# Kernel tuning notes

Measured on AMD Instinct MI355X. Metric: run time of the kernel, lower is better.

## Reference

```python
import jax, jax.numpy as jnp
import numpy as np

N = 50000
E = 800000
F_IN = 128
HID = 16
HEADS = 8
C = 16
NEG_SLOPE = 0.2


def setup_inputs() -> dict:
    key = jax.random.key(0)
    ks = jax.random.split(key, 12)
    glorot = lambda k, shape: jax.random.normal(k, shape, jnp.float32) * jnp.sqrt(2.0 / (shape[0] + shape[-1]))
    return {
        "x": jax.random.normal(ks[0], (N, F_IN), jnp.float32),
        "edge_index": jax.random.randint(ks[1], (2, E), 0, N, jnp.int32),
        "x2": jax.random.normal(ks[2], (N, F_IN), jnp.float32),
        "edge_index2": jax.random.randint(ks[3], (2, E), 0, N, jnp.int32),
        # conv1: GATConv(F_IN -> HID, heads=HEADS, concat=True)
        "W1": glorot(ks[4], (F_IN, HEADS * HID)),
        "a1_src": glorot(ks[5], (HEADS, HID)),
        "a1_dst": glorot(ks[6], (HEADS, HID)),
        "b1": jnp.zeros((HEADS * HID,), jnp.float32),
        # conv2: GATConv(HEADS*HID -> C, heads=1, concat=False)
        "W2": glorot(ks[7], (HEADS * HID, 1 * C)),
        "a2_src": glorot(ks[8], (1, C)),
        "a2_dst": glorot(ks[9], (1, C)),
        "b2": jnp.zeros((C,), jnp.float32),
    }


def gat_conv(x, edge_index, W, a_src, a_dst, bias, concat):
    """PyG-style GATConv with self-loops, segment softmax over destinations."""
    n = x.shape[0]
    heads, out = a_src.shape
    h = (x @ W).reshape(n, heads, out)               # [N, H, O]
    loops = jnp.arange(n, dtype=edge_index.dtype)
    src = jnp.concatenate([edge_index[0], loops])     # messages flow src -> dst
    dst = jnp.concatenate([edge_index[1], loops])
    alpha_s = jnp.einsum('nho,ho->nh', h, a_src)
    alpha_d = jnp.einsum('nho,ho->nh', h, a_dst)
    e = jax.nn.leaky_relu(alpha_s[src] + alpha_d[dst], NEG_SLOPE)  # [E+N, H]
    m = jax.lax.stop_gradient(jax.ops.segment_max(e, dst, num_segments=n))
    w = jnp.exp(e - m[dst])
    denom = jax.ops.segment_sum(w, dst, num_segments=n)
    alpha = w / (denom[dst] + 1e-16)                  # segment softmax
    msg = h[src] * alpha[:, :, None]                  # [E+N, H, O]
    agg = jax.ops.segment_sum(msg, dst, num_segments=n)
    agg = agg.reshape(n, heads * out) if concat else agg.mean(axis=1)
    return agg + bias


def forward_once(x, edge_index, W1, a1_src, a1_dst, b1, W2, a2_src, a2_dst, b2):
    # dropout(p=0.6) is identity in eval mode
    h = jax.nn.elu(gat_conv(x, edge_index, W1, a1_src, a1_dst, b1, concat=True))
    return gat_conv(h, edge_index, W2, a2_src, a2_dst, b2, concat=False)


def reference(x, edge_index, x2, edge_index2, W1, a1_src, a1_dst, b1, W2, a2_src, a2_dst, b2):
    y = forward_once(x, edge_index, W1, a1_src, a1_dst, b1, W2, a2_src, a2_dst, b2)
    z = forward_once(x2, edge_index2, W1, a1_src, a1_dst, b1, W2, a2_src, a2_dst, b2)
    eps = 1e-8
    ny = jnp.maximum(jnp.linalg.norm(y, axis=1), eps)
    nz = jnp.maximum(jnp.linalg.norm(z, axis=1), eps)
    cos = jnp.sum(y * z, axis=1) / (ny * nz)
    ls_y = jax.nn.log_softmax(y, axis=1)
    ls_z = jax.nn.log_softmax(z, axis=1)
    return (ls_y, 1.0 - cos, ls_z, ls_y, ls_y)
```

## Files before the change

### kernel.cpp

```cpp
#include <hip/hip_runtime.h>
#include <hip/hip_bf16.h>

#define N_NODES 50000
#define N_EDGES 800000
#define F_INS   128
#define HIDDEN  16
#define HEADS   8
#define HO      128
#define C_OUT   16
#define NEG_SLOPE 0.2f
#define SLOT    64
#define NB_G1   ((N_NODES + 63) / 64)
#define NB_GAT1 ((N_NODES + 3) / 4)
#define NB_G2   ((N_NODES + 16) / 16)

#define NP      50016
#define AS_ST   ((size_t)NP * 8)
#define H1B_ST  ((size_t)NP * 64)
#define HL1_ST  ((size_t)N_NODES * 64)
#define H2_ST   ((size_t)NP * 16)
#define AS2_ST  ((size_t)NP)

#define NCLS     128
#define CLS_MUL  1342u
#define CLS_SH   19
#define CAP      8192
#define CHUNK    2048
#define NB_BKT   ((N_EDGES + CHUNK - 1) / CHUNK)
#define GPAD     16

typedef unsigned short u16;
typedef unsigned int   u32;
typedef int v4i __attribute__((ext_vector_type(4)));
typedef short bf16x8 __attribute__((ext_vector_type(8)));
typedef float f32x4 __attribute__((ext_vector_type(4)));

__device__ __forceinline__ float bf2f(u16 u) {
    union { u32 i; float f; } t; t.i = ((u32)u) << 16; return t.f;
}
__device__ __forceinline__ float bflo(u32 q) {
    union { u32 i; float f; } t; t.i = q << 16; return t.f;
}
__device__ __forceinline__ float bfhi(u32 q) {
    union { u32 i; float f; } t; t.i = q & 0xFFFF0000u; return t.f;
}
__device__ __forceinline__ u32 f2bf(float f) {
    union { float f; u32 i; } t; t.f = f;
    u32 x = t.i;
    u32 lsb = (x >> 16) & 1u;
    x += 0x7FFFu + lsb;
    return x >> 16;
}
__device__ __forceinline__ u32 cvtpk(float lo, float hi) {
    u32 r;
    asm("v_cvt_pk_bf16_f32 %0, %1, %2" : "=v"(r) : "v"(lo), "v"(hi));
    return r;
}
__device__ __forceinline__ float lrelu(float t) {
    return fmaxf(t, NEG_SLOPE * t);
}
__device__ __forceinline__ int cls_of(int d) { return (int)(((u32)d * CLS_MUL) >> CLS_SH); }
__host__ __device__ __forceinline__ int cls_base(int c) { return (int)(((u32)c * 524288u + (CLS_MUL - 1)) / CLS_MUL); }

__global__ void k_wt(const float* __restrict__ W1, const float* __restrict__ a1s,
                     const float* __restrict__ a1d, u32* __restrict__ w1t,
                     u32* __restrict__ a1t, int* __restrict__ gcur) {
    int t = threadIdx.x;
    if (blockIdx.x < 32) {
        int e = blockIdx.x * 256 + t;
        int c = e >> 6, kp = e & 63;
        float lo = W1[(2 * kp) * 128 + c];
        float hi = W1[(2 * kp + 1) * 128 + c];
        w1t[e] = (f2bf(hi) << 16) | f2bf(lo);
    } else {
        #pragma unroll
        for (int i = 0; i < GPAD; ++i) gcur[t * GPAD + i] = 0;
        #pragma unroll
        for (int i = 0; i < 4; ++i) {
            int wi = t + i * 256;
            int n = wi >> 6, kp = wi & 63;
            int h = n >> 1;
            const float* av = ((n & 1) ? a1d : a1s) + h * 16;
            float s0 = 0.f, s1 = 0.f;
            #pragma unroll
            for (int c = 0; c < 16; ++c) {
                s0 += W1[(2 * kp) * 128 + h * 16 + c] * av[c];
                s1 += W1[(2 * kp + 1) * 128 + h * 16 + c] * av[c];
            }
            a1t[wi] = (f2bf(s1) << 16) | f2bf(s0);
        }
    }
}

__launch_bounds__(256)
__global__ void k_bg1(const int* __restrict__ ei0, const int* __restrict__ ei1,
                      int* __restrict__ gcur, u32* __restrict__ bucket,
                      const float* __restrict__ x1g, const float* __restrict__ x2g,
                      const u32* __restrict__ w1t, const u32* __restrict__ a1t,
                      u32* __restrict__ h1b, float* __restrict__ as_,
                      float* __restrict__ ad_) {
    __shared__ int cnt[NCLS];
    __shared__ int bse[NCLS];
    int t = threadIdx.x;

    if (blockIdx.x < 2 * NB_BKT) {
        int g = blockIdx.x & 1;
        int chunk = blockIdx.x >> 1;
        int e0 = chunk * CHUNK + t * 8;
        bool act = e0 < N_EDGES;

        if (t < NCLS) cnt[t] = 0;
        __syncthreads();

        const int* src = g ? ei1 : ei0;
        const int* dst = src + N_EDGES;
        int d8[8], s8[8], c8[8];
        if (act) {
            v4i da = *(const v4i*)(dst + e0), db = *(const v4i*)(dst + e0 + 4);
            v4i sa = *(const v4i*)(src + e0), sb = *(const v4i*)(src + e0 + 4);
            d8[0]=da[0]; d8[1]=da[1]; d8[2]=da[2]; d8[3]=da[3];
            d8[4]=db[0]; d8[5]=db[1]; d8[6]=db[2]; d8[7]=db[3];
            s8[0]=sa[0]; s8[1]=sa[1]; s8[2]=sa[2]; s8[3]=sa[3];
            s8[4]=sb[0]; s8[5]=sb[1]; s8[6]=sb[2]; s8[7]=sb[3];
            #pragma unroll
            for (int j = 0; j < 8; ++j) {
                c8[j] = cls_of(d8[j]);
                atomicAdd(&cnt[c8[j]], 1);
            }
        }
        __syncthreads();
        if (t < NCLS) {
            int n = cnt[t];
            bse[t] = n ? atomicAdd(&gcur[(g * NCLS + t) * GPAD], n) : 0;
            cnt[t] = 0;
        }
        __syncthreads();
        if (act) {
            #pragma unroll
            for (int j = 0; j < 8; ++j) {
                int c = c8[j];
                int p = atomicAdd(&cnt[c], 1);
                bucket[(size_t)(g * NCLS + c) * CAP + bse[c] + p] =
                    ((u32)d8[j] << 16) | (u32)s8[j];
            }
        }
        return;
    }

    int bid = blockIdx.x - 2 * NB_BKT;
    int g = bid >= NB_G1;
    if (g) bid -= NB_G1;
    const float* x = g ? x2g : x1g;
    u32*   h1o = h1b + (size_t)g * H1B_ST;
    float* aso = as_ + (size_t)g * AS_ST;
    float* ado = ad_ + (size_t)g * AS_ST;
    int r0 = bid * 64;

    int lane = t & 63;
    int wid = t >> 6;
    int n = lane & 15, quad = lane >> 4;

    int r = r0 + wid * 16 + n;
    bool rok = r < N_NODES;
    const float4* xr = (const float4*)(x + (size_t)r * 128);
    float4 xf[8];
    #pragma unroll
    for (int kt = 0; kt < 4; ++kt) {
        int cb = kt * 8 + quad * 2;
        xf[kt * 2]     = rok ? xr[cb]     : make_float4(0.f, 0.f, 0.f, 0.f);
        xf[kt * 2 + 1] = rok ? xr[cb + 1] : make_float4(0.f, 0.f, 0.f, 0.f);
    }

    f32x4 acc[8], acca;
    #pragma unroll
    for (int ct = 0; ct < 8; ++ct) acc[ct] = (f32x4){0.f, 0.f, 0.f, 0.f};
    acca = (f32x4){0.f, 0.f, 0.f, 0.f};

    #pragma unroll
    for (int kt = 0; kt < 4; ++kt) {
        union { uint4 u; bf16x8 v; } af;
        float4 f0 = xf[kt * 2], f1 = xf[kt * 2 + 1];
        af.u.x = cvtpk(f0.x, f0.y);
        af.u.y = cvtpk(f0.z, f0.w);
        af.u.z = cvtpk(f1.x, f1.y);
        af.u.w = cvtpk(f1.z, f1.w);
        #pragma unroll
        for (int ct = 0; ct < 8; ++ct) {
            union { uint4 u; bf16x8 v; } bf_;
            bf_.u = *(const uint4*)(w1t + (ct * 16 + n) * 64 + kt * 16 + quad * 4);
            acc[ct] = __builtin_amdgcn_mfma_f32_16x16x32_bf16(af.v, bf_.v, acc[ct], 0, 0, 0);
        }
        union { uint4 u; bf16x8 v; } ba;
        ba.u = *(const uint4*)(a1t + n * 64 + kt * 16 + quad * 4);
        acca = __builtin_amdgcn_mfma_f32_16x16x32_bf16(af.v, ba.v, acca, 0, 0, 0);
    }

    int h = n >> 1;
    #pragma unroll
    for (int reg = 0; reg < 4; ++reg) {
        int gr = r0 + wid * 16 + quad * 4 + reg;
        bool ok = gr <= N_NODES;
        float av = (gr == N_NODES) ? -1e30f : acca[reg];
        if (ok) {
            if (n & 1) ado[gr * 8 + h] = av;
            else       aso[gr * 8 + h] = av;
        }
        #pragma unroll
        for (int ct = 0; ct < 8; ++ct) {
            float ot = __shfl_xor(acc[ct][reg], 1);
            if (!(n & 1) && ok)
                h1o[(size_t)gr * 64 + ct * 8 + (n >> 1)] = cvtpk(acc[ct][reg], ot);
        }
    }
}

__launch_bounds__(1024)
__global__ void k_build(const int* __restrict__ gcur, const u32* __restrict__ bucket,
                        int* __restrict__ cursor, u16* __restrict__ col) {
    __shared__ int cnt[391];
    __shared__ __align__(16) u16 scol[391 * SLOT];
    int t = threadIdx.x;
    int c = blockIdx.x & (NCLS - 1);
    int g = blockIdx.x >> 7;
    int d0 = cls_base(c);
    int d1 = (c == NCLS - 1) ? N_NODES : cls_base(c + 1);
    int nn = d1 - d0;
    for (int j = t; j < nn; j += 1024) cnt[j] = 0;
    __syncthreads();

    int size = gcur[(g * NCLS + c) * GPAD];
    const u32* bp = bucket + (size_t)(g * NCLS + c) * CAP;
    for (int i = t; i < size; i += 1024) {
        u32 e = bp[i];
        int d = (int)(e >> 16);
        int s = (int)(e & 0xFFFFu);
        int p = atomicAdd(&cnt[d - d0], 1);
        if (p < SLOT) scol[(d - d0) * SLOT + p] = (u16)s;
    }
    __syncthreads();
    int* cur = cursor + g * N_NODES;
    for (int j = t; j < nn; j += 1024) {
        int raw = cnt[j];
        int n0 = min(raw, SLOT);
        int n1 = (n0 + 7) & ~7;
        for (int p = n0; p < n1; ++p) scol[j * SLOT + p] = (u16)N_NODES;
        cur[d0 + j] = raw;
    }
    __syncthreads();
    uint4* dst = (uint4*)(col + ((size_t)g * N_NODES + d0) * SLOT);
    const uint4* srcv = (const uint4*)scol;
    int n16 = nn * 8;
    for (int i = t; i < n16; i += 1024) dst[i] = srcv[i];
}

#define GAT1_ISSUE(I, q0,q1,q2,q3,q4,q5,q6,q7, A) do { \
    u32 ix_=(I).x, iy_=(I).y, iz_=(I).z, iw_=(I).w; \
    q0 = *(const u32*)(h1c + (((ix_ & 0xFFFFu) << 8) | lane4)); \
    q1 = *(const u32*)(h1c + (((ix_ >> 16)     << 8) | lane4)); \
    q2 = *(const u32*)(h1c + (((iy_ & 0xFFFFu) << 8) | lane4)); \
    q3 = *(const u32*)(h1c + (((iy_ >> 16)     << 8) | lane4)); \
    q4 = *(const u32*)(h1c + (((iz_ & 0xFFFFu) << 8) | lane4)); \
    q5 = *(const u32*)(h1c + (((iz_ >> 16)     << 8) | lane4)); \
    q6 = *(const u32*)(h1c + (((iw_ & 0xFFFFu) << 8) | lane4)); \
    q7 = *(const u32*)(h1c + (((iw_ >> 16)     << 8) | lane4)); \
    u32 ds_ = (j8 & 4) ? ((j8 & 2) ? iw_ : iz_) : ((j8 & 2) ? iy_ : ix_); \
    u32 sA_ = (j8 & 1) ? (ds_ >> 16) : (ds_ & 0xFFFFu); \
    A = *(const float*)(asc + ((sA_ << 5) | ha4)); \
} while (0)

#define GAT1_CONS(q0,q1,q2,q3,q4,q5,q6,q7, A) do { \
    int wli_ = __float_as_int(__expf(lrelu((A) + ad_a))); \
    float w0 = __int_as_float(__builtin_amdgcn_ds_bpermute(vb,       wli_)); \
    float w1 = __int_as_float(__builtin_amdgcn_ds_bpermute(vb + 32,  wli_)); \
    float w2 = __int_as_float(__builtin_amdgcn_ds_bpermute(vb + 64,  wli_)); \
    float w3 = __int_as_float(__builtin_amdgcn_ds_bpermute(vb + 96,  wli_)); \
    float w4 = __int_as_float(__builtin_amdgcn_ds_bpermute(vb + 128, wli_)); \
    float w5 = __int_as_float(__builtin_amdgcn_ds_bpermute(vb + 160, wli_)); \
    float w6 = __int_as_float(__builtin_amdgcn_ds_bpermute(vb + 192, wli_)); \
    float w7 = __int_as_float(__builtin_amdgcn_ds_bpermute(vb + 224, wli_)); \
    denom += ((w0 + w1) + (w2 + w3)) + ((w4 + w5) + (w6 + w7)); \
    ax += w0 * bflo(q0) + w1 * bflo(q1) + w2 * bflo(q2) + w3 * bflo(q3) \
        + w4 * bflo(q4) + w5 * bflo(q5) + w6 * bflo(q6) + w7 * bflo(q7); \
    ay += w0 * bfhi(q0) + w1 * bfhi(q1) + w2 * bfhi(q2) + w3 * bfhi(q3) \
        + w4 * bfhi(q4) + w5 * bfhi(q5) + w6 * bfhi(q6) + w7 * bfhi(q7); \
} while (0)

__launch_bounds__(256)
__global__ void k_gat1(const u32* __restrict__ h1b, const float* __restrict__ as_,
                       const float* __restrict__ ad_, const int* __restrict__ cursor,
                       const u16* __restrict__ col, const float* __restrict__ b1,
                       u32* __restrict__ hL1) {
    int t = threadIdx.x;
    int lane = t & 63;
    int bid = blockIdx.x;
    int g = bid >= NB_GAT1;
    if (g) bid -= NB_GAT1;
    int node = bid * 4 + (t >> 6);

    const char*  h1c = (const char*)(h1b + (size_t)g * H1B_ST);
    const char*  asc = (const char*)(as_ + (size_t)g * AS_ST);
    const float* ad1 = ad_ + (size_t)g * AS_ST;
    const u16*   cp  = col + ((size_t)g * N_NODES + node) * SLOT;

    int hc = lane >> 3;
    int ha = lane & 7;
    int j8 = lane >> 3;
    int vb = hc << 2;
    u32 lane4 = (u32)lane << 2;
    u32 ha4 = (u32)ha << 2;

    float ad_a = ad1[node * 8 + ha];
    float as_c = as_[(size_t)g * AS_ST + node * 8 + hc];
    float ad_c = ad1[node * 8 + hc];

    float w = __expf(lrelu(as_c + ad_c));
    float denom = w;
    u32 q = *(const u32*)(h1c + (((u32)node << 8) | lane4));
    float ax = w * bflo(q), ay = w * bfhi(q);

    int deg = min(cursor[g * N_NODES + node], SLOT);
    int nb = (deg + 7) >> 3;
    if (nb) {
        u32 qa0,qa1,qa2,qa3,qa4,qa5,qa6,qa7;
        u32 qb0,qb1,qb2,qb3,qb4,qb5,qb6,qb7;
        float Aa, Ab;
        uint4 Ia, Ib;
        Ia = *(const uint4*)cp;
        GAT1_ISSUE(Ia, qa0,qa1,qa2,qa3,qa4,qa5,qa6,qa7, Aa);
        if (nb > 1) {
            Ib = *(const uint4*)(cp + 8);
            GAT1_ISSUE(Ib, qb0,qb1,qb2,qb3,qb4,qb5,qb6,qb7, Ab);
        }
        int b = 0;
        for (;;) {
            GAT1_CONS(qa0,qa1,qa2,qa3,qa4,qa5,qa6,qa7, Aa);
            if (++b >= nb) break;
            if (b + 1 < nb) {
                Ia = *(const uint4*)(cp + (b + 1) * 8);
                GAT1_ISSUE(Ia, qa0,qa1,qa2,qa3,qa4,qa5,qa6,qa7, Aa);
            }
            GAT1_CONS(qb0,qb1,qb2,qb3,qb4,qb5,qb6,qb7, Ab);
            if (++b >= nb) break;
            if (b + 1 < nb) {
                Ib = *(const uint4*)(cp + (b + 1) * 8);
                GAT1_ISSUE(Ib, qb0,qb1,qb2,qb3,qb4,qb5,qb6,qb7, Ab);
            }
        }
    }
    float inv = 1.f / (denom + 1e-16f);
    int c = lane * 2;
    float o0 = ax * inv + b1[c];
    float o1 = ay * inv + b1[c + 1];
    o0 = (o0 > 0.f) ? o0 : (__expf(o0) - 1.f);
    o1 = (o1 > 0.f) ? o1 : (__expf(o1) - 1.f);
    hL1[(size_t)g * HL1_ST + (size_t)node * 64 + lane] = cvtpk(o0, o1);
}

__launch_bounds__(256)
__global__ void k_gemm2(const u32* __restrict__ hL1, const float* __restrict__ W2,
                        const float* __restrict__ a2s, const float* __restrict__ a2d,
                        float* __restrict__ h2, float* __restrict__ as2,
                        float* __restrict__ ad2) {
    __shared__ float w2s[F_INS * C_OUT];
    __shared__ float hs[16 * 136];
    int t = threadIdx.x;
    int bid = blockIdx.x;
    int g = bid >= NB_G2;
    if (g) bid -= NB_G2;
    const u16* hL = (const u16*)(hL1 + (size_t)g * HL1_ST);
    float* h2o  = h2  + (size_t)g * H2_ST;
    float* as2o = as2 + (size_t)g * AS2_ST;
    float* ad2o = ad2 + (size_t)g * AS2_ST;

    const float4* w4 = (const float4*)W2;
    #pragma unroll
    for (int i = 0; i < 2; ++i) {
        int idx = t + i * 256;
        ((float4*)w2s)[idx] = w4[idx];
    }
    int r0 = bid * 16;
    const ushort4* hg = (const ushort4*)hL;
    #pragma unroll
    for (int i = 0; i < 2; ++i) {
        int idx = t + i * 256;
        int r  = idx >> 5;
        int c4 = idx & 31;
        ushort4 qq = make_ushort4(0, 0, 0, 0);
        if (r0 + r < N_NODES) qq = hg[(size_t)(r0 + r) * 32 + c4];
        float4 v; v.x = bf2f(qq.x); v.y = bf2f(qq.y); v.z = bf2f(qq.z); v.w = bf2f(qq.w);
        *(float4*)(hs + r * 136 + c4 * 4) = v;
    }
    __syncthreads();

    int c = t & 15, r = t >> 4;
    float acc = 0.f;
    #pragma unroll 8
    for (int k = 0; k < F_INS; ++k) acc += hs[r * 136 + k] * w2s[k * C_OUT + c];
    int n = r0 + r;
    if (n <= N_NODES) h2o[(size_t)n * C_OUT + c] = acc;

    float sa = acc * a2s[c];
    float sd = acc * a2d[c];
    #pragma unroll
    for (int m = 1; m < 16; m <<= 1) {
        sa += __shfl_xor(sa, m);
        sd += __shfl_xor(sd, m);
    }
    if (c == 0 && n <= N_NODES) {
        as2o[n] = (n == N_NODES) ? -1e30f : sa;
        ad2o[n] = sd;
    }
}

#define G2_ISSUE(I, H2C, ASC, v0,v1,v2,v3,v4,v5,v6,v7, A) do { \
    u32 ix_=(I).x, iy_=(I).y, iz_=(I).z, iw_=(I).w; \
    v0 = *(const float*)((H2C) + (((ix_ & 0xFFFFu) << 6) | c4)); \
    v1 = *(const float*)((H2C) + (((ix_ >> 16)     << 6) | c4)); \
    v2 = *(const float*)((H2C) + (((iy_ & 0xFFFFu) << 6) | c4)); \
    v3 = *(const float*)((H2C) + (((iy_ >> 16)     << 6) | c4)); \
    v4 = *(const float*)((H2C) + (((iz_ & 0xFFFFu) << 6) | c4)); \
    v5 = *(const float*)((H2C) + (((iz_ >> 16)     << 6) | c4)); \
    v6 = *(const float*)((H2C) + (((iw_ & 0xFFFFu) << 6) | c4)); \
    v7 = *(const float*)((H2C) + (((iw_ >> 16)     << 6) | c4)); \
    u32 ds_ = (jsel & 4) ? ((jsel & 2) ? iw_ : iz_) : ((jsel & 2) ? iy_ : ix_); \
    u32 sA_ = (jsel & 1) ? (ds_ >> 16) : (ds_ & 0xFFFFu); \
    A = *(const float*)((ASC) + (sA_ << 2)); \
} while (0)

#define G2_CONS(v0,v1,v2,v3,v4,v5,v6,v7, A, AD, DEN, ACC) do { \
    int wli_ = __float_as_int(__expf(lrelu((A) + (AD)))); \
    float w0 = __int_as_float(__builtin_amdgcn_ds_bpermute(gb,      wli_)); \
    float w1 = __int_as_float(__builtin_amdgcn_ds_bpermute(gb + 4,  wli_)); \
    float w2 = __int_as_float(__builtin_amdgcn_ds_bpermute(gb + 8,  wli_)); \
    float w3 = __int_as_float(__builtin_amdgcn_ds_bpermute(gb + 12, wli_)); \
    float w4 = __int_as_float(__builtin_amdgcn_ds_bpermute(gb + 16, wli_)); \
    float w5 = __int_as_float(__builtin_amdgcn_ds_bpermute(gb + 20, wli_)); \
    float w6 = __int_as_float(__builtin_amdgcn_ds_bpermute(gb + 24, wli_)); \
    float w7 = __int_as_float(__builtin_amdgcn_ds_bpermute(gb + 28, wli_)); \
    DEN += ((w0 + w1) + (w2 + w3)) + ((w4 + w5) + (w6 + w7)); \
    ACC += (w0 * v0 + w1 * v1 + w2 * v2 + w3 * v3) \
         + (w4 * v4 + w5 * v5 + w6 * v6 + w7 * v7); \
} while (0)

__launch_bounds__(256)
__global__ void k_gat2e(const float* __restrict__ h2, const float* __restrict__ as2,
                        const float* __restrict__ ad2, const int* __restrict__ cursor,
                        const u16* __restrict__ col, const float* __restrict__ b2,
                        float* __restrict__ out) {
    int t = threadIdx.x;
    int node = blockIdx.x * 16 + (t >> 4);
    int c = t & 15;
    int lane = t & 63;
    u32 c4 = (u32)c << 2;
    int jsel = lane & 7;
    u32 gb = (u32)(lane & 48) << 2;
    float b2c = b2[c];

    const char* h2Y = (const char*)h2;
    const char* h2Z = (const char*)(h2 + H2_ST);
    const char* asY = (const char*)as2;
    const char* asZ = (const char*)(as2 + AS2_ST);
    const u16* cpY = col + (size_t)node * SLOT;
    const u16* cpZ = col + ((size_t)N_NODES + node) * SLOT;
    float adY = ad2[node];
    float adZ = ad2[AS2_ST + node];

    float wY = __expf(lrelu(*(const float*)(asY + ((u32)node << 2)) + adY));
    float dY = wY;
    float aY = wY * *(const float*)(h2Y + (((u32)node << 6) | c4));
    float wZ = __expf(lrelu(*(const float*)(asZ + ((u32)node << 2)) + adZ));
    float dZ = wZ;
    float aZ = wZ * *(const float*)(h2Z + (((u32)node << 6) | c4));

    int nbY = (min(cursor[node], SLOT) + 7) >> 3;
    int nbZ = (min(cursor[N_NODES + node], SLOT) + 7) >> 3;

    float y0,y1,y2,y3,y4,y5,y6,y7, Ay;
    float z0,z1,z2,z3,z4,z5,z6,z7, Az;
    uint4 I;
    if (nbY) { I = *(const uint4*)cpY; G2_ISSUE(I, h2Y, asY, y0,y1,y2,y3,y4,y5,y6,y7, Ay); }
    if (nbZ) { I = *(const uint4*)cpZ; G2_ISSUE(I, h2Z, asZ, z0,z1,z2,z3,z4,z5,z6,z7, Az); }
    int bY = 0, bZ = 0;
    while (bY < nbY || bZ < nbZ) {
        if (bY < nbY) {
            G2_CONS(y0,y1,y2,y3,y4,y5,y6,y7, Ay, adY, dY, aY);
            ++bY;
            if (bY < nbY) {
                I = *(const uint4*)(cpY + bY * 8);
                G2_ISSUE(I, h2Y, asY, y0,y1,y2,y3,y4,y5,y6,y7, Ay);
            }
        }
        if (bZ < nbZ) {
            G2_CONS(z0,z1,z2,z3,z4,z5,z6,z7, Az, adZ, dZ, aZ);
            ++bZ;
            if (bZ < nbZ) {
                I = *(const uint4*)(cpZ + bZ * 8);
                G2_ISSUE(I, h2Z, asZ, z0,z1,z2,z3,z4,z5,z6,z7, Az);
            }
        }
    }
    float yv = aY / (dY + 1e-16f) + b2c;
    float zv = aZ / (dZ + 1e-16f) + b2c;

    float my = yv, mz = zv;
    #pragma unroll
    for (int m = 1; m < 16; m <<= 1) {
        my = fmaxf(my, __shfl_xor(my, m));
        mz = fmaxf(mz, __shfl_xor(mz, m));
    }
    float sy = __expf(yv - my), sz = __expf(zv - mz);
    float dot = yv * zv, ny = yv * yv, nz = zv * zv;
    #pragma unroll
    for (int m = 1; m < 16; m <<= 1) {
        sy  += __shfl_xor(sy, m);
        sz  += __shfl_xor(sz, m);
        dot += __shfl_xor(dot, m);
        ny  += __shfl_xor(ny, m);
        nz  += __shfl_xor(nz, m);
    }
    float lsey = my + __logf(sy);
    float lsez = mz + __logf(sz);
    float omc = 1.f - dot / (fmaxf(sqrtf(ny), 1e-8f) * fmaxf(sqrtf(nz), 1e-8f));

    const int O1 = N_NODES * C_OUT;
    const int O2 = O1 + N_NODES;
    const int O3 = O2 + N_NODES * C_OUT;
    const int O4 = O3 + N_NODES * C_OUT;
    float ly = yv - lsey;
    float lz = zv - lsez;
    int base = node * 16 + c;
    out[base]      = ly;
    out[O2 + base] = lz;
    out[O3 + base] = ly;
    out[O4 + base] = ly;
    if (c == 0) out[O1 + node] = omc;
}

extern "C" void kernel_launch(void* const* d_in, const int* in_sizes, int n_in,
                              void* d_out, int out_size, void* d_ws, size_t ws_size,
                              hipStream_t stream) {
    (void)in_sizes; (void)n_in; (void)out_size; (void)ws_size;
    const float* x1  = (const float*)d_in[0];
    const int*   ei1 = (const int*)d_in[1];
    const float* x2  = (const float*)d_in[2];
    const int*   ei2 = (const int*)d_in[3];
    const float* W1  = (const float*)d_in[4];
    const float* a1s = (const float*)d_in[5];
    const float* a1d = (const float*)d_in[6];
    const float* b1  = (const float*)d_in[7];
    const float* W2  = (const float*)d_in[8];
    const float* a2s = (const float*)d_in[9];
    const float* a2d = (const float*)d_in[10];
    const float* b2  = (const float*)d_in[11];
    float* out = (float*)d_out;

    char* p = (char*)d_ws;
    int* gcur      = (int*)p; p += (size_t)2 * NCLS * GPAD * 4;
    u32* w1t       = (u32*)p; p += (size_t)128 * 64 * 4;
    u32* a1t       = (u32*)p; p += (size_t)16 * 64 * 4;
    int* cursor    = (int*)p; p += (size_t)2 * N_NODES * 4;
    u16* col       = (u16*)p; p += (size_t)2 * N_NODES * SLOT * 2;
    float* as1  = (float*)p; p += (size_t)2 * AS_ST * 4;
    float* ad1  = (float*)p; p += (size_t)2 * AS_ST * 4;
    float* h2   = (float*)p; p += (size_t)2 * H2_ST * 4;
    float* as2  = (float*)p; p += (size_t)2 * AS2_ST * 4;
    float* ad2  = (float*)p; p += (size_t)2 * AS2_ST * 4;
    u32* hL1    = (u32*)p;   p += (size_t)2 * HL1_ST * 4;
    u32* h1b    = (u32*)p;   p += (size_t)2 * H1B_ST * 4;
    u32* bucket = hL1;

    k_wt    <<<33, 256, 0, stream>>>(W1, a1s, a1d, w1t, a1t, gcur);
    k_bg1   <<<2 * NB_BKT + 2 * NB_G1, 256, 0, stream>>>(ei1, ei2, gcur, bucket,
                                                         x1, x2, w1t, a1t, h1b, as1, ad1);
    k_build <<<2 * NCLS, 1024, 0, stream>>>(gcur, bucket, cursor, col);
    k_gat1  <<<2 * NB_GAT1, 256, 0, stream>>>(h1b, as1, ad1, cursor, col, b1, hL1);
    k_gemm2 <<<2 * NB_G2, 256, 0, stream>>>(hL1, W2, a2s, a2d, h2, as2, ad2);
    k_gat2e <<<N_NODES / 16, 256, 0, stream>>>(h2, as2, ad2, cursor, col, b2, out);
}
```

Baseline: 291.5 us.

## Fuse second-layer linear projection into first GAT aggregation kernel

Removes the separate k_gemm2 kernel and its intermediate bf16 hL1 buffer. Each wavefront computes the 128→16 projection of its node's ELU output in registers, using ds_bpermute to broadcast features against a transposed W2 prepared in k_wt, then writes h2 and the layer-2 attention scalars directly. This saves one launch plus a global write and read of the hidden activations. In exchange k_gat1 does more per-node work and register pressure, and a dedicated extra block initialises the padding row.

```diff
diff --git a/kernel.cpp b/kernel.cpp
--- a/kernel.cpp
+++ b/kernel.cpp
@@ -12,12 +12,10 @@
 #define SLOT    64
 #define NB_G1   ((N_NODES + 63) / 64)
 #define NB_GAT1 ((N_NODES + 3) / 4)
-#define NB_G2   ((N_NODES + 16) / 16)
 
 #define NP      50016
 #define AS_ST   ((size_t)NP * 8)
 #define H1B_ST  ((size_t)NP * 64)
-#define HL1_ST  ((size_t)N_NODES * 64)
 #define H2_ST   ((size_t)NP * 16)
 #define AS2_ST  ((size_t)NP)
 
@@ -63,8 +61,9 @@
 __host__ __device__ __forceinline__ int cls_base(int c) { return (int)(((u32)c * 524288u + (CLS_MUL - 1)) / CLS_MUL); }
 
 __global__ void k_wt(const float* __restrict__ W1, const float* __restrict__ a1s,
-                     const float* __restrict__ a1d, u32* __restrict__ w1t,
-                     u32* __restrict__ a1t, int* __restrict__ gcur) {
+                     const float* __restrict__ a1d, const float* __restrict__ W2,
+                     u32* __restrict__ w1t, u32* __restrict__ a1t,
+                     float* __restrict__ w2t, int* __restrict__ gcur) {
     int t = threadIdx.x;
     if (blockIdx.x < 32) {
         int e = blockIdx.x * 256 + t;
@@ -75,6 +74,12 @@
     } else {
         #pragma unroll
         for (int i = 0; i < GPAD; ++i) gcur[t * GPAD + i] = 0;
+        #pragma unroll
+        for (int i = 0; i < 8; ++i) {
+            int idx = t * 8 + i;
+            int c = idx >> 7, k = idx & 127;
+            w2t[idx] = W2[k * 16 + c];
+        }
         #pragma unroll
         for (int i = 0; i < 4; ++i) {
             int wi = t + i * 256;
@@ -286,13 +291,26 @@
 } while (0)
 
 __launch_bounds__(256)
-__global__ void k_gat1(const u32* __restrict__ h1b, const float* __restrict__ as_,
-                       const float* __restrict__ ad_, const int* __restrict__ cursor,
-                       const u16* __restrict__ col, const float* __restrict__ b1,
-                       u32* __restrict__ hL1) {
+__global__ void k_gat1f(const u32* __restrict__ h1b, const float* __restrict__ as_,
+                        const float* __restrict__ ad_, const int* __restrict__ cursor,
+                        const u16* __restrict__ col, const float* __restrict__ b1,
+                        const float* __restrict__ w2t, const float* __restrict__ a2s,
+                        const float* __restrict__ a2d, float* __restrict__ h2,
+                        float* __restrict__ as2, float* __restrict__ ad2) {
     int t = threadIdx.x;
     int lane = t & 63;
     int bid = blockIdx.x;
+    if (bid == 2 * NB_GAT1) {
+        if (t < 32) {
+            int g = t >> 4, c = t & 15;
+            h2[(size_t)g * H2_ST + (size_t)N_NODES * 16 + c] = 0.f;
+            if (c == 0) {
+                as2[(size_t)g * AS2_ST + N_NODES] = -1e30f;
+                ad2[(size_t)g * AS2_ST + N_NODES] = 0.f;
+            }
+        }
+        return;
+    }
     int g = bid >= NB_GAT1;
     if (g) bid -= NB_GAT1;
     int node = bid * 4 + (t >> 6);
@@ -301,6 +319,9 @@
     const char*  asc = (const char*)(as_ + (size_t)g * AS_ST);
     const float* ad1 = ad_ + (size_t)g * AS_ST;
     const u16*   cp  = col + ((size_t)g * N_NODES + node) * SLOT;
+    float* h2o  = h2  + (size_t)g * H2_ST;
+    float* as2o = as2 + (size_t)g * AS2_ST;
+    float* ad2o = ad2 + (size_t)g * AS2_ST;
 
     int hc = lane >> 3;
     int ha = lane & 7;
@@ -348,68 +369,36 @@
         }
     }
     float inv = 1.f / (denom + 1e-16f);
-    int c = lane * 2;
-    float o0 = ax * inv + b1[c];
-    float o1 = ay * inv + b1[c + 1];
+    int c2 = lane * 2;
+    float o0 = ax * inv + b1[c2];
+    float o1 = ay * inv + b1[c2 + 1];
     o0 = (o0 > 0.f) ? o0 : (__expf(o0) - 1.f);
     o1 = (o1 > 0.f) ? o1 : (__expf(o1) - 1.f);
-    hL1[(size_t)g * HL1_ST + (size_t)node * 64 + lane] = cvtpk(o0, o1);
-}
-
-__launch_bounds__(256)
-__global__ void k_gemm2(const u32* __restrict__ hL1, const float* __restrict__ W2,
-                        const float* __restrict__ a2s, const float* __restrict__ a2d,
-                        float* __restrict__ h2, float* __restrict__ as2,
-                        float* __restrict__ ad2) {
-    __shared__ float w2s[F_INS * C_OUT];
-    __shared__ float hs[16 * 136];
-    int t = threadIdx.x;
-    int bid = blockIdx.x;
-    int g = bid >= NB_G2;
-    if (g) bid -= NB_G2;
-    const u16* hL = (const u16*)(hL1 + (size_t)g * HL1_ST);
-    float* h2o  = h2  + (size_t)g * H2_ST;
-    float* as2o = as2 + (size_t)g * AS2_ST;
-    float* ad2o = ad2 + (size_t)g * AS2_ST;
-
-    const float4* w4 = (const float4*)W2;
-    #pragma unroll
-    for (int i = 0; i < 2; ++i) {
-        int idx = t + i * 256;
-        ((float4*)w2s)[idx] = w4[idx];
-    }
-    int r0 = bid * 16;
-    const ushort4* hg = (const ushort4*)hL;
-    #pragma unroll
-    for (int i = 0; i < 2; ++i) {
-        int idx = t + i * 256;
-        int r  = idx >> 5;
-        int c4 = idx & 31;
-        ushort4 qq = make_ushort4(0, 0, 0, 0);
-        if (r0 + r < N_NODES) qq = hg[(size_t)(r0 + r) * 32 + c4];
-        float4 v; v.x = bf2f(qq.x); v.y = bf2f(qq.y); v.z = bf2f(qq.z); v.w = bf2f(qq.w);
-        *(float4*)(hs + r * 136 + c4 * 4) = v;
-    }
-    __syncthreads();
-
-    int c = t & 15, r = t >> 4;
-    float acc = 0.f;
-    #pragma unroll 8
-    for (int k = 0; k < F_INS; ++k) acc += hs[r * 136 + k] * w2s[k * C_OUT + c];
-    int n = r0 + r;
-    if (n <= N_NODES) h2o[(size_t)n * C_OUT + c] = acc;
-
-    float sa = acc * a2s[c];
-    float sd = acc * a2d[c];
+    u32 q2 = cvtpk(o0, o1);
+
+    int cc = lane & 15, seg = lane >> 4;
+    const float4* wr = (const float4*)(w2t + cc * 128 + seg * 32);
+    float acc2 = 0.f;
+    #pragma unroll
+    for (int kq = 0; kq < 8; ++kq) {
+        float4 wv = wr[kq];
+        u32 qv0 = (u32)__builtin_amdgcn_ds_bpermute((seg * 16 + kq * 2) << 2, (int)q2);
+        u32 qv1 = (u32)__builtin_amdgcn_ds_bpermute((seg * 16 + kq * 2 + 1) << 2, (int)q2);
+        acc2 += bflo(qv0) * wv.x + bfhi(qv0) * wv.y
+              + bflo(qv1) * wv.z + bfhi(qv1) * wv.w;
+    }
+    acc2 += __shfl_xor(acc2, 16);
+    acc2 += __shfl_xor(acc2, 32);
+    if (lane < 16) h2o[(u32)node * 16 + cc] = acc2;
+
+    float sa = acc2 * a2s[cc];
+    float sd = acc2 * a2d[cc];
     #pragma unroll
     for (int m = 1; m < 16; m <<= 1) {
         sa += __shfl_xor(sa, m);
         sd += __shfl_xor(sd, m);
     }
-    if (c == 0 && n <= N_NODES) {
-        as2o[n] = (n == N_NODES) ? -1e30f : sa;
-        ad2o[n] = sd;
-    }
+    if (lane == 0) { as2o[node] = sa; ad2o[node] = sd; }
 }
 
 #define G2_ISSUE(I, H2C, ASC, v0,v1,v2,v3,v4,v5,v6,v7, A) do { \
@@ -558,6 +547,7 @@
     int* gcur      = (int*)p; p += (size_t)2 * NCLS * GPAD * 4;
     u32* w1t       = (u32*)p; p += (size_t)128 * 64 * 4;
     u32* a1t       = (u32*)p; p += (size_t)16 * 64 * 4;
+    float* w2t     = (float*)p; p += (size_t)16 * 128 * 4;
     int* cursor    = (int*)p; p += (size_t)2 * N_NODES * 4;
     u16* col       = (u16*)p; p += (size_t)2 * N_NODES * SLOT * 2;
     float* as1  = (float*)p; p += (size_t)2 * AS_ST * 4;
@@ -565,15 +555,14 @@
     float* h2   = (float*)p; p += (size_t)2 * H2_ST * 4;
     float* as2  = (float*)p; p += (size_t)2 * AS2_ST * 4;
     float* ad2  = (float*)p; p += (size_t)2 * AS2_ST * 4;
-    u32* hL1    = (u32*)p;   p += (size_t)2 * HL1_ST * 4;
+    u32* bucket = (u32*)p;   p += (size_t)2 * NCLS * CAP * 4;
     u32* h1b    = (u32*)p;   p += (size_t)2 * H1B_ST * 4;
-    u32* bucket = hL1;
-
-    k_wt    <<<33, 256, 0, stream>>>(W1, a1s, a1d, w1t, a1t, gcur);
+
+    k_wt    <<<33, 256, 0, stream>>>(W1, a1s, a1d, W2, w1t, a1t, w2t, gcur);
     k_bg1   <<<2 * NB_BKT + 2 * NB_G1, 256, 0, stream>>>(ei1, ei2, gcur, bucket,
                                                          x1, x2, w1t, a1t, h1b, as1, ad1);
     k_build <<<2 * NCLS, 1024, 0, stream>>>(gcur, bucket, cursor, col);
-    k_gat1  <<<2 * NB_GAT1, 256, 0, stream>>>(h1b, as1, ad1, cursor, col, b1, hL1);
-    k_gemm2 <<<2 * NB_G2, 256, 0, stream>>>(hL1, W2, a2s, a2d, h2, as2, ad2);
+    k_gat1f <<<2 * NB_GAT1 + 1, 256, 0, stream>>>(h1b, as1, ad1, cursor, col, b1,
+                                                  w2t, a2s, a2d, h2, as2, ad2);
     k_gat2e <<<N_NODES / 16, 256, 0, stream>>>(h2, as2, ad2, cursor, col, b2, out);
 }
```

After: 332.1 us. 1.14x slower.
